# Performance work log

Hardware: AMD Instinct MI355X
Metric: run time of the kernel (lower is better)

Reference implementation:

```python
import jax, jax.numpy as jnp
import numpy as np

N_QUBITS = 10
DEPTH = 3
KSIZE = 16
DILATION = 1
NFREQ = 8

I4 = np.eye(4, dtype=np.complex64)
XX4 = np.fliplr(np.eye(4)).astype(np.complex64)
YY4 = np.array([[0, 0, 0, -1], [0, 0, 1, 0], [0, 1, 0, 0], [-1, 0, 0, 0]], dtype=np.complex64)


def _u3(t, p, l):
    ct = jnp.cos(t / 2).astype(jnp.complex64)
    st = jnp.sin(t / 2).astype(jnp.complex64)
    ep, el = jnp.exp(1j * p), jnp.exp(1j * l)
    return jnp.stack([jnp.stack([ct, -el * st]), jnp.stack([ep * st, ep * el * ct])])


def _ising_zz(t):
    em, ep = jnp.exp(-0.5j * t), jnp.exp(0.5j * t)
    return jnp.diag(jnp.stack([em, ep, ep, em]))


def _ising_xx(t):
    return jnp.cos(t / 2) * I4 - 1j * jnp.sin(t / 2) * XX4


def _ising_yy(t):
    return jnp.cos(t / 2) * I4 - 1j * jnp.sin(t / 2) * YY4


def _cu3(t, p, l):
    # controlled-U3 (control = 1): deferred-measurement form of qml.cond(measure, U3)
    return jnp.eye(4, dtype=jnp.complex64).at[2:, 2:].set(_u3(t, p, l))


def _apply_1q(state, U, wire):
    s = jnp.moveaxis(state, 1 + wire, -1)
    if U.ndim == 3:  # per-sample gate (batched angles)
        s = jnp.einsum('bij,b...j->b...i', U, s)
    else:
        s = jnp.einsum('ij,...j->...i', U, s)
    return jnp.moveaxis(s, -1, 1 + wire)


def _apply_2q(state, U, w1, w2):
    s = jnp.moveaxis(state, (1 + w1, 1 + w2), (-2, -1))
    shp = s.shape
    s = s.reshape(shp[:-2] + (4,))
    s = jnp.einsum('ij,...j->...i', U, s)
    return jnp.moveaxis(s.reshape(shp), (-2, -1), (1 + w1, 1 + w2))


def _run_circuit(angles, freq_scale, conv_params, pool_params):
    Bm = angles.shape[0]
    state = jnp.zeros((Bm, 2 ** N_QUBITS), jnp.complex64).at[:, 0].set(1.0)
    state = state.reshape((Bm,) + (2,) * N_QUBITS)
    # frequency-matched encoding: RY(a) then RX(freq_scale * a), per-sample angles
    for i in range(N_QUBITS):
        a = angles[:, i]
        c = jnp.cos(a / 2).astype(jnp.complex64)
        s = jnp.sin(a / 2).astype(jnp.complex64)
        ry = jnp.stack([jnp.stack([c, -s], -1), jnp.stack([s, c], -1)], -2)
        state = _apply_1q(state, ry, i)
        b = freq_scale[i] * a
        cb = jnp.cos(b / 2).astype(jnp.complex64)
        sb = jnp.sin(b / 2).astype(jnp.complex64)
        rx = jnp.stack([jnp.stack([cb, -1j * sb], -1), jnp.stack([-1j * sb, cb], -1)], -2)
        state = _apply_1q(state, rx, i)
    wires = list(range(N_QUBITS))
    for layer in range(DEPTH):
        wp = conv_params[layer]
        nw = len(wires)
        for parity in (0, 1):
            for i2, w in enumerate(wires):
                if i2 % 2 == parity and i2 < nw - 1:
                    nxt = wires[i2 + 1]
                    state = _apply_1q(state, _u3(wp[i2, 0], wp[i2, 1], wp[i2, 2]), w)
                    state = _apply_1q(state, _u3(wp[i2 + 1, 3], wp[i2 + 1, 4], wp[i2 + 1, 5]), nxt)
                    state = _apply_2q(state, _ising_zz(wp[i2, 6]), w, nxt)
                    state = _apply_2q(state, _ising_yy(wp[i2, 7]), w, nxt)
                    state = _apply_2q(state, _ising_xx(wp[i2, 8]), w, nxt)
                    state = _apply_1q(state, _u3(wp[i2, 9], wp[i2, 10], wp[i2, 11]), w)
                    state = _apply_1q(state, _u3(wp[i2 + 1, 12], wp[i2 + 1, 13], wp[i2 + 1, 14]), nxt)
        pp = pool_params[layer]
        for i2, w in enumerate(wires):
            if i2 % 2 == 1:
                state = _apply_2q(state, _cu3(pp[i2 // 2, 0], pp[i2 // 2, 1], pp[i2 // 2, 2]), w, wires[i2 - 1])
        wires = wires[::2]
    p = jnp.abs(state) ** 2
    p = p.reshape(Bm, 2, -1).sum(-1)
    return p[:, 0] - p[:, 1]  # <Z_0>


def _forward(x, proj_w, proj_b, freq_scale, conv_params, pool_params, agg_weights):
    B, C, T = x.shape
    eff = DILATION * (KSIZE - 1)
    W = T - eff
    idx = jnp.arange(W)[:, None] + DILATION * jnp.arange(KSIZE)[None, :]  # [W,K]
    win = x[:, :, idx]  # [B,C,W,K]
    f = jnp.fft.rfft(win, axis=-1)[..., :NFREQ]  # [B,C,W,NF]
    feats = jnp.stack([jnp.log1p(jnp.abs(f)), jnp.angle(f) / jnp.pi], -1)  # [B,C,W,NF,2]
    feats = jnp.transpose(feats, (0, 2, 1, 3, 4)).reshape(B, W, -1)  # [B,W,C*NF*2]
    proj = jnp.tanh(feats @ proj_w.T + proj_b) * jnp.pi  # [B,W,n_qubits]
    ev = _run_circuit(proj.reshape(B * W, N_QUBITS), freq_scale, conv_params, pool_params)
    outs = ev.reshape(B, W)
    wts = jax.nn.softmax(agg_weights[:W])
    return (outs * wts[None, :]).sum(1)


def setup_inputs():
    key = jax.random.key(0)
    k = jax.random.split(key, 6)
    fft_dim = 22 * NFREQ * 2
    return {
        'x': jax.random.normal(k[0], (16, 22, 128), jnp.float32),
        'proj_w': jax.random.normal(k[1], (N_QUBITS, fft_dim), jnp.float32) / np.sqrt(fft_dim).astype(np.float32),
        'proj_b': jnp.zeros((N_QUBITS,), jnp.float32),
        'freq_scale': jnp.linspace(0.5, 3.0, N_QUBITS, dtype=jnp.float32),
        'conv_params': 0.1 * jax.random.normal(k[2], (DEPTH, N_QUBITS, 15), jnp.float32),
        'pool_params': 0.1 * jax.random.normal(k[3], (DEPTH, N_QUBITS // 2, 3), jnp.float32),
        'agg_weights': jnp.zeros((113,), jnp.float32),
    }


def reference(x, proj_w, proj_b, freq_scale, conv_params, pool_params, agg_weights):
    return _forward(x, proj_w, proj_b, freq_scale, conv_params, pool_params, agg_weights)
```

## Files before the change

### kernel.cpp

```cpp
#include <hip/hip_runtime.h>
#include <math.h>

#define NQ 10
#define NSTATE 1024
#define WW 113
#define BB 16
#define CC 22
#define KK 16
#define NF 8
#define FDIM 352
#define NS (BB*WW)
#define NGATE 23

__device__ __forceinline__ float2 cmul(float2 a, float2 b) {
    return make_float2(a.x*b.x - a.y*b.y, a.x*b.y + a.y*b.x);
}

__constant__ int G_KIND[NGATE]  = {0,0,0,0,0, 0,0,0,0, 1,1,1,1,1, 0,0,0,0, 1,1, 0,0, 1};
__constant__ int G_LAYER[NGATE] = {0,0,0,0,0, 0,0,0,0, 0,0,0,0,0, 1,1,1,1, 1,1, 2,2, 2};
__constant__ int G_IA[NGATE]    = {0,2,4,6,8, 1,3,5,7, 0,1,2,3,4, 0,2,1,3, 0,1, 0,1, 0};

__device__ void u3mat(float2* U, float th, float ph, float lm) {
    float ct, st, cp, sp, cl, sl;
    sincosf(th * 0.5f, &st, &ct);
    sincosf(ph, &sp, &cp);
    sincosf(lm, &sl, &cl);
    U[0] = make_float2(ct, 0.f);
    U[1] = make_float2(-cl * st, -sl * st);
    U[2] = make_float2(cp * st, sp * st);
    U[3] = make_float2((cp * cl - sp * sl) * ct, (sp * cl + cp * sl) * ct);
}

__device__ void mm4(float2* C, const float2* A, const float2* B) {
#pragma unroll
    for (int i = 0; i < 4; ++i)
#pragma unroll
        for (int j = 0; j < 4; ++j) {
            float2 acc = make_float2(0.f, 0.f);
#pragma unroll
            for (int k = 0; k < 4; ++k) {
                float2 p = cmul(A[i*4+k], B[k*4+j]);
                acc.x += p.x; acc.y += p.y;
            }
            C[i*4+j] = acc;
        }
}

__global__ __launch_bounds__(64) void matgen_kernel(
    const float* __restrict__ conv,
    const float* __restrict__ pool,
    float2* __restrict__ mats)
{
    int g = threadIdx.x;
    if (g >= NGATE) return;
    int kind = G_KIND[g], layer = G_LAYER[g], ia = G_IA[g];
    float2 F[16];
    if (kind == 0) {
        const float* wp = conv + layer * 150;
        float2 Uw0[4], Un0[4], Uw1[4], Un1[4];
        u3mat(Uw0, wp[ia*15+0], wp[ia*15+1], wp[ia*15+2]);
        u3mat(Un0, wp[(ia+1)*15+3], wp[(ia+1)*15+4], wp[(ia+1)*15+5]);
        u3mat(Uw1, wp[ia*15+9], wp[ia*15+10], wp[ia*15+11]);
        u3mat(Un1, wp[(ia+1)*15+12], wp[(ia+1)*15+13], wp[(ia+1)*15+14]);
        float2 Kpre[16], Kpost[16];
#pragma unroll
        for (int a = 0; a < 2; ++a)
#pragma unroll
        for (int b = 0; b < 2; ++b)
#pragma unroll
        for (int c = 0; c < 2; ++c)
#pragma unroll
        for (int d = 0; d < 2; ++d) {
            Kpre [(2*a+b)*4 + (2*c+d)] = cmul(Uw0[a*2+c], Un0[b*2+d]);
            Kpost[(2*a+b)*4 + (2*c+d)] = cmul(Uw1[a*2+c], Un1[b*2+d]);
        }
        float cz, sz, cy, sy, cx, sx;
        sincosf(wp[ia*15+6] * 0.5f, &sz, &cz);
        sincosf(wp[ia*15+7] * 0.5f, &sy, &cy);
        sincosf(wp[ia*15+8] * 0.5f, &sx, &cx);
        float2 Z[16], Y[16], X[16];
#pragma unroll
        for (int k = 0; k < 16; ++k) { Z[k] = make_float2(0,0); Y[k] = make_float2(0,0); X[k] = make_float2(0,0); }
        Z[0]  = make_float2(cz, -sz); Z[5]  = make_float2(cz, sz);
        Z[10] = make_float2(cz,  sz); Z[15] = make_float2(cz, -sz);
        Y[0] = Y[5] = Y[10] = Y[15] = make_float2(cy, 0);
        Y[0*4+3] = make_float2(0,  sy); Y[1*4+2] = make_float2(0, -sy);
        Y[2*4+1] = make_float2(0, -sy); Y[3*4+0] = make_float2(0,  sy);
        X[0] = X[5] = X[10] = X[15] = make_float2(cx, 0);
        X[0*4+3] = X[1*4+2] = X[2*4+1] = X[3*4+0] = make_float2(0, -sx);
        float2 T1[16], M[16], T2[16];
        mm4(T1, Y, Z);
        mm4(M, X, T1);
        mm4(T2, M, Kpre);
        mm4(F, Kpost, T2);
    } else {
        const float* pp = pool + layer * 15 + ia * 3;
        float2 U[4];
        u3mat(U, pp[0], pp[1], pp[2]);
#pragma unroll
        for (int k = 0; k < 16; ++k) F[k] = make_float2(0,0);
        F[0*4+0] = make_float2(1,0); F[1*4+1] = make_float2(1,0);
        F[2*4+2] = U[0]; F[2*4+3] = U[1];
        F[3*4+2] = U[2]; F[3*4+3] = U[3];
    }
#pragma unroll
    for (int k = 0; k < 16; ++k) mats[g*16 + k] = F[k];
}

template<int PW, int PN>
__device__ __forceinline__ void gate2q(float* sre, float* sim, const float2* m, int tid)
{
    constexpr int PL = (PW < PN) ? PW : PN;
    constexpr int PH = (PW < PN) ? PN : PW;
    int t1   = ((tid >> PL) << (PL + 1)) | (tid & ((1 << PL) - 1));
    int base = ((t1  >> PH) << (PH + 1)) | (t1  & ((1 << PH) - 1));
    const int i0 = base;
    const int i1 = base | (1 << PN);
    const int i2 = base | (1 << PW);
    const int i3 = base | (1 << PW) | (1 << PN);
    float ar[4], ai[4];
    ar[0] = sre[i0]; ai[0] = sim[i0];
    ar[1] = sre[i1]; ai[1] = sim[i1];
    ar[2] = sre[i2]; ai[2] = sim[i2];
    ar[3] = sre[i3]; ai[3] = sim[i3];
    float nr[4], ni[4];
#pragma unroll
    for (int g = 0; g < 4; ++g) {
        float accr = 0.f, acci = 0.f;
#pragma unroll
        for (int h = 0; h < 4; ++h) {
            float2 mm = m[g*4 + h];
            accr += mm.x * ar[h] - mm.y * ai[h];
            acci += mm.x * ai[h] + mm.y * ar[h];
        }
        nr[g] = accr; ni[g] = acci;
    }
    sre[i0] = nr[0]; sim[i0] = ni[0];
    sre[i1] = nr[1]; sim[i1] = ni[1];
    sre[i2] = nr[2]; sim[i2] = ni[2];
    sre[i3] = nr[3]; sim[i3] = ni[3];
}

__global__ __launch_bounds__(256) void fused_kernel(
    const float* __restrict__ x,
    const float* __restrict__ proj_w,
    const float* __restrict__ proj_b,
    const float* __restrict__ freq_scale,
    const float2* __restrict__ mats_g,
    float* __restrict__ ev)
{
    const int s = blockIdx.x;
    const int b = s / WW, w = s % WW;
    const int tid = threadIdx.x;

    __shared__ float sre[NSTATE], sim[NSTATE];
    __shared__ float2 smats[NGATE * 16];
    __shared__ float twre[16], twim[16];
    __shared__ float angs[NQ];
    __shared__ float2 vq[2 * NQ];
    __shared__ float part[4];

    float* win  = sre;
    float* feat = sim;

    for (int e = tid; e < NGATE * 16; e += 256) smats[e] = mats_g[e];
    for (int e = tid; e < CC * KK; e += 256) {
        int c = e >> 4, n = e & 15;
        win[e] = x[b * (CC * 128) + c * 128 + w + n];
    }
    if (tid < 16) {
        float ang = -(float)M_PI * (float)tid / 8.0f;
        twre[tid] = cosf(ang);
        twim[tid] = sinf(ang);
    }
    __syncthreads();

    if (tid < CC * NF) {
        int c = tid >> 3, k = tid & 7;
        float re = 0.f, im = 0.f;
#pragma unroll
        for (int n = 0; n < 16; ++n) {
            int m = (k * n) & 15;
            float xv = win[c * 16 + n];
            re += xv * twre[m];
            im += xv * twim[m];
        }
        feat[c * 16 + k * 2]     = log1pf(sqrtf(re * re + im * im));
        feat[c * 16 + k * 2 + 1] = atan2f(im, re) * (float)(1.0 / M_PI);
    }
    __syncthreads();

    {
        int v = tid >> 6, lane = tid & 63;
        for (int q = v; q < NQ; q += 4) {
            float acc = 0.f;
            for (int e = lane; e < FDIM; e += 64) acc += feat[e] * proj_w[q * FDIM + e];
            for (int off = 32; off > 0; off >>= 1) acc += __shfl_xor(acc, off);
            if (lane == 0) angs[q] = tanhf(acc + proj_b[q]) * (float)M_PI;
        }
    }
    __syncthreads();

    if (tid < NQ) {
        float a = angs[tid];
        float bf = freq_scale[tid] * a;
        float ca, sa, cb, sb;
        sincosf(a * 0.5f, &sa, &ca);
        sincosf(bf * 0.5f, &sb, &cb);
        vq[2 * tid]     = make_float2(cb * ca, -sb * sa);
        vq[2 * tid + 1] = make_float2(cb * sa, -sb * ca);
    }
    __syncthreads();

    for (int idx = tid; idx < NSTATE; idx += 256) {
        float r = 1.f, i = 0.f;
#pragma unroll
        for (int q = 0; q < NQ; ++q) {
            int bit = (idx >> (9 - q)) & 1;
            float2 vv = vq[2 * q + bit];
            float nr = r * vv.x - i * vv.y;
            float ni = r * vv.y + i * vv.x;
            r = nr; i = ni;
        }
        sre[idx] = r; sim[idx] = i;
    }
    __syncthreads();

#define GATE(G, PW, PN) gate2q<PW, PN>(sre, sim, smats + (G)*16, tid); __syncthreads();
    GATE(0, 9, 8) GATE(1, 7, 6) GATE(2, 5, 4) GATE(3, 3, 2) GATE(4, 1, 0)
    GATE(5, 8, 7) GATE(6, 6, 5) GATE(7, 4, 3) GATE(8, 2, 1)
    GATE(9, 8, 9) GATE(10, 6, 7) GATE(11, 4, 5) GATE(12, 2, 3) GATE(13, 0, 1)
    GATE(14, 9, 7) GATE(15, 5, 3) GATE(16, 7, 5) GATE(17, 3, 1)
    GATE(18, 7, 9) GATE(19, 3, 5)
    GATE(20, 9, 5) GATE(21, 5, 1)
    GATE(22, 5, 9)
#undef GATE

    float local = 0.f;
    for (int idx = tid; idx < NSTATE; idx += 256) {
        float r = sre[idx], i = sim[idx];
        float p = r * r + i * i;
        local += (idx < 512) ? p : -p;
    }
    for (int off = 32; off > 0; off >>= 1) local += __shfl_xor(local, off);
    if ((tid & 63) == 0) part[tid >> 6] = local;
    __syncthreads();
    if (tid == 0) ev[s] = part[0] + part[1] + part[2] + part[3];
}

__global__ __launch_bounds__(64) void agg_kernel(
    const float* __restrict__ ev,
    const float* __restrict__ aggw,
    float* __restrict__ out)
{
    const int t = threadIdx.x;
    float a0 = (t < WW) ? aggw[t] : -1e30f;
    float a1 = (t + 64 < WW) ? aggw[t + 64] : -1e30f;
    float m = fmaxf(a0, a1);
    for (int off = 32; off > 0; off >>= 1) m = fmaxf(m, __shfl_xor(m, off));
    float e0 = (t < WW) ? expf(a0 - m) : 0.f;
    float e1 = (t + 64 < WW) ? expf(a1 - m) : 0.f;
    float es = e0 + e1;
    for (int off = 32; off > 0; off >>= 1) es += __shfl_xor(es, off);
    float inv = 1.0f / es;
    for (int b = 0; b < BB; ++b) {
        float acc = 0.f;
        if (t < WW) acc += ev[b * WW + t] * e0;
        if (t + 64 < WW) acc += ev[b * WW + t + 64] * e1;
        for (int off = 32; off > 0; off >>= 1) acc += __shfl_xor(acc, off);
        if (t == 0) out[b] = acc * inv;
    }
}

extern "C" void kernel_launch(void* const* d_in, const int* in_sizes, int n_in,
                              void* d_out, int out_size, void* d_ws, size_t ws_size,
                              hipStream_t stream)
{
    const float* x           = (const float*)d_in[0];
    const float* proj_w      = (const float*)d_in[1];
    const float* proj_b      = (const float*)d_in[2];
    const float* freq_scale  = (const float*)d_in[3];
    const float* conv_params = (const float*)d_in[4];
    const float* pool_params = (const float*)d_in[5];
    const float* aggw        = (const float*)d_in[6];
    float* out = (float*)d_out;

    float2* mats = (float2*)d_ws;
    float* ev = (float*)d_ws + NGATE * 16 * 2;

    matgen_kernel<<<1, 64, 0, stream>>>(conv_params, pool_params, mats);
    fused_kernel<<<NS, 256, 0, stream>>>(x, proj_w, proj_b, freq_scale, mats, ev);
    agg_kernel<<<1, 64, 0, stream>>>(ev, aggw, out);
}
```

Measured before the change: 131.2 us.

## Fuse softmax aggregation into main kernel via atomics and swizzle interleaved state

Moves the softmax weight computation into the prep kernel and replaces the separate aggregation kernel with a per-block atomicAdd of the weighted expectation value. This removes one launch and the intermediate ev buffer. The state vector becomes an interleaved float2 array with an XOR swizzle to reduce LDS bank conflicts, and gate matrices are read straight from global memory instead of being staged in shared memory. The changes lower LDS footprint and launch overhead, at the cost of atomic contention on 16 outputs and nondeterministic summation order.

Measured after the change: 112.0 us. 14.6% less time.

```diff
diff --git a/kernel.cpp b/kernel.cpp
--- a/kernel.cpp
+++ b/kernel.cpp
@@ -11,6 +11,7 @@
 #define FDIM 352
 #define NS (BB*WW)
 #define NGATE 23
+#define SL(j) ((j) ^ (((j) >> 5) & 31))
 
 __device__ __forceinline__ float2 cmul(float2 a, float2 b) {
     return make_float2(a.x*b.x - a.y*b.y, a.x*b.y + a.y*b.x);
@@ -46,14 +47,31 @@
         }
 }
 
-__global__ __launch_bounds__(64) void matgen_kernel(
+__global__ __launch_bounds__(64) void prep_kernel(
     const float* __restrict__ conv,
     const float* __restrict__ pool,
-    float2* __restrict__ mats)
-{
-    int g = threadIdx.x;
-    if (g >= NGATE) return;
-    int kind = G_KIND[g], layer = G_LAYER[g], ia = G_IA[g];
+    const float* __restrict__ aggw,
+    float2* __restrict__ mats,
+    float* __restrict__ wts,
+    float* __restrict__ out)
+{
+    const int t = threadIdx.x;
+
+    float a0 = (t < WW) ? aggw[t] : -1e30f;
+    float a1 = (t + 64 < WW) ? aggw[t + 64] : -1e30f;
+    float mx = fmaxf(a0, a1);
+    for (int off = 32; off > 0; off >>= 1) mx = fmaxf(mx, __shfl_xor(mx, off));
+    float e0 = (t < WW) ? expf(a0 - mx) : 0.f;
+    float e1 = (t + 64 < WW) ? expf(a1 - mx) : 0.f;
+    float es = e0 + e1;
+    for (int off = 32; off > 0; off >>= 1) es += __shfl_xor(es, off);
+    float inv = 1.0f / es;
+    if (t < WW) wts[t] = e0 * inv;
+    if (t + 64 < WW) wts[t + 64] = e1 * inv;
+    if (t < BB) out[t] = 0.f;
+
+    if (t >= NGATE) return;
+    int kind = G_KIND[t], layer = G_LAYER[t], ia = G_IA[t];
     float2 F[16];
     if (kind == 0) {
         const float* wp = conv + layer * 150;
@@ -104,41 +122,37 @@
         F[3*4+2] = U[2]; F[3*4+3] = U[3];
     }
 #pragma unroll
-    for (int k = 0; k < 16; ++k) mats[g*16 + k] = F[k];
+    for (int k = 0; k < 16; ++k) mats[t*16 + k] = F[k];
 }
 
 template<int PW, int PN>
-__device__ __forceinline__ void gate2q(float* sre, float* sim, const float2* m, int tid)
+__device__ __forceinline__ void gate2q(float2* st, const float2* __restrict__ m, int tid)
 {
     constexpr int PL = (PW < PN) ? PW : PN;
     constexpr int PH = (PW < PN) ? PN : PW;
     int t1   = ((tid >> PL) << (PL + 1)) | (tid & ((1 << PL) - 1));
     int base = ((t1  >> PH) << (PH + 1)) | (t1  & ((1 << PH) - 1));
-    const int i0 = base;
-    const int i1 = base | (1 << PN);
-    const int i2 = base | (1 << PW);
-    const int i3 = base | (1 << PW) | (1 << PN);
-    float ar[4], ai[4];
-    ar[0] = sre[i0]; ai[0] = sim[i0];
-    ar[1] = sre[i1]; ai[1] = sim[i1];
-    ar[2] = sre[i2]; ai[2] = sim[i2];
-    ar[3] = sre[i3]; ai[3] = sim[i3];
-    float nr[4], ni[4];
+    const int i0 = SL(base);
+    const int i1 = SL(base | (1 << PN));
+    const int i2 = SL(base | (1 << PW));
+    const int i3 = SL(base | (1 << PW) | (1 << PN));
+    float2 a[4];
+    a[0] = st[i0]; a[1] = st[i1]; a[2] = st[i2]; a[3] = st[i3];
+    float2 n[4];
 #pragma unroll
     for (int g = 0; g < 4; ++g) {
-        float accr = 0.f, acci = 0.f;
+        float accx = 0.f, accy = 0.f;
 #pragma unroll
         for (int h = 0; h < 4; ++h) {
             float2 mm = m[g*4 + h];
-            accr += mm.x * ar[h] - mm.y * ai[h];
-            acci += mm.x * ai[h] + mm.y * ar[h];
-        }
-        nr[g] = accr; ni[g] = acci;
-    }
-    sre[i0] = nr[0]; sim[i0] = ni[0];
-    sre[i1] = nr[1]; sim[i1] = ni[1];
-    sre[i2] = nr[2]; sim[i2] = ni[2];
-    sre[i3] = nr[3]; sim[i3] = ni[3];
+            accx = fmaf(mm.x, a[h].x, accx);
+            accx = fmaf(-mm.y, a[h].y, accx);
+            accy = fmaf(mm.x, a[h].y, accy);
+            accy = fmaf(mm.y, a[h].x, accy);
+        }
+        n[g] = make_float2(accx, accy);
+    }
+    st[i0] = n[0]; st[i1] = n[1]; st[i2] = n[2]; st[i3] = n[3];
 }
 
 __global__ __launch_bounds__(256) void fused_kernel(
@@ -146,24 +160,23 @@
     const float* __restrict__ proj_w,
     const float* __restrict__ proj_b,
     const float* __restrict__ freq_scale,
-    const float2* __restrict__ mats_g,
-    float* __restrict__ ev)
+    const float2* __restrict__ mats,
+    const float* __restrict__ wts,
+    float* __restrict__ out)
 {
     const int s = blockIdx.x;
     const int b = s / WW, w = s % WW;
     const int tid = threadIdx.x;
 
-    __shared__ float sre[NSTATE], sim[NSTATE];
-    __shared__ float2 smats[NGATE * 16];
+    __shared__ float2 st[NSTATE];
     __shared__ float twre[16], twim[16];
     __shared__ float angs[NQ];
     __shared__ float2 vq[2 * NQ];
     __shared__ float part[4];
 
-    float* win  = sre;
-    float* feat = sim;
-
-    for (int e = tid; e < NGATE * 16; e += 256) smats[e] = mats_g[e];
+    float* win  = (float*)st;
+    float* feat = (float*)st + 512;
+
     for (int e = tid; e < CC * KK; e += 256) {
         int c = e >> 4, n = e & 15;
         win[e] = x[b * (CC * 128) + c * 128 + w + n];
@@ -175,6 +188,7 @@
     }
     __syncthreads();
 
+    float fval = 0.f, fval2 = 0.f;
     if (tid < CC * NF) {
         int c = tid >> 3, k = tid & 7;
         float re = 0.f, im = 0.f;
@@ -185,8 +199,14 @@
             re += xv * twre[m];
             im += xv * twim[m];
         }
-        feat[c * 16 + k * 2]     = log1pf(sqrtf(re * re + im * im));
-        feat[c * 16 + k * 2 + 1] = atan2f(im, re) * (float)(1.0 / M_PI);
+        fval  = log1pf(sqrtf(re * re + im * im));
+        fval2 = atan2f(im, re) * (float)(1.0 / M_PI);
+    }
+    __syncthreads();
+    if (tid < CC * NF) {
+        int c = tid >> 3, k = tid & 7;
+        feat[c * 16 + k * 2]     = fval;
+        feat[c * 16 + k * 2 + 1] = fval2;
     }
     __syncthreads();
 
@@ -222,11 +242,11 @@
             float ni = r * vv.y + i * vv.x;
             r = nr; i = ni;
         }
-        sre[idx] = r; sim[idx] = i;
-    }
-    __syncthreads();
-
-#define GATE(G, PW, PN) gate2q<PW, PN>(sre, sim, smats + (G)*16, tid); __syncthreads();
+        st[SL(idx)] = make_float2(r, i);
+    }
+    __syncthreads();
+
+#define GATE(G, PW, PN) gate2q<PW, PN>(st, mats + (G)*16, tid); __syncthreads();
     GATE(0, 9, 8) GATE(1, 7, 6) GATE(2, 5, 4) GATE(3, 3, 2) GATE(4, 1, 0)
     GATE(5, 8, 7) GATE(6, 6, 5) GATE(7, 4, 3) GATE(8, 2, 1)
     GATE(9, 8, 9) GATE(10, 6, 7) GATE(11, 4, 5) GATE(12, 2, 3) GATE(13, 0, 1)
@@ -238,37 +258,16 @@
 
     float local = 0.f;
     for (int idx = tid; idx < NSTATE; idx += 256) {
-        float r = sre[idx], i = sim[idx];
-        float p = r * r + i * i;
+        float2 am = st[idx];
+        float p = am.x * am.x + am.y * am.y;
         local += (idx < 512) ? p : -p;
     }
     for (int off = 32; off > 0; off >>= 1) local += __shfl_xor(local, off);
     if ((tid & 63) == 0) part[tid >> 6] = local;
     __syncthreads();
-    if (tid == 0) ev[s] = part[0] + part[1] + part[2] + part[3];
-}
-
-__global__ __launch_bounds__(64) void agg_kernel(
-    const float* __restrict__ ev,
-    const float* __restrict__ aggw,
-    float* __restrict__ out)
-{
-    const int t = threadIdx.x;
-    float a0 = (t < WW) ? aggw[t] : -1e30f;
-    float a1 = (t + 64 < WW) ? aggw[t + 64] : -1e30f;
-    float m = fmaxf(a0, a1);
-    for (int off = 32; off > 0; off >>= 1) m = fmaxf(m, __shfl_xor(m, off));
-    float e0 = (t < WW) ? expf(a0 - m) : 0.f;
-    float e1 = (t + 64 < WW) ? expf(a1 - m) : 0.f;
-    float es = e0 + e1;
-    for (int off = 32; off > 0; off >>= 1) es += __shfl_xor(es, off);
-    float inv = 1.0f / es;
-    for (int b = 0; b < BB; ++b) {
-        float acc = 0.f;
-        if (t < WW) acc += ev[b * WW + t] * e0;
-        if (t + 64 < WW) acc += ev[b * WW + t + 64] * e1;
-        for (int off = 32; off > 0; off >>= 1) acc += __shfl_xor(acc, off);
-        if (t == 0) out[b] = acc * inv;
+    if (tid == 0) {
+        float ev = part[0] + part[1] + part[2] + part[3];
+        atomicAdd(&out[b], ev * wts[w]);
     }
 }
 
@@ -286,9 +285,8 @@
     float* out = (float*)d_out;
 
     float2* mats = (float2*)d_ws;
-    float* ev = (float*)d_ws + NGATE * 16 * 2;
-
-    matgen_kernel<<<1, 64, 0, stream>>>(conv_params, pool_params, mats);
-    fused_kernel<<<NS, 256, 0, stream>>>(x, proj_w, proj_b, freq_scale, mats, ev);
-    agg_kernel<<<1, 64, 0, stream>>>(ev, aggw, out);
-}
+    float* wts   = (float*)d_ws + NGATE * 16 * 2;
+
+    prep_kernel<<<1, 64, 0, stream>>>(conv_params, pool_params, aggw, mats, wts, out);
+    fused_kernel<<<NS, 256, 0, stream>>>(x, proj_w, proj_b, freq_scale, mats, wts, out);
+}
```
